# Performance work log

Hardware: AMD Instinct MI355X
Metric: run time of the kernel (lower is better)

Reference implementation:

```python
import jax, jax.numpy as jnp
import numpy as np

B, T, TM, V = 16, 128, 128, 25
CIN, CM = 64, 256
H, D1, D2 = 8, 32, 32
COUT, K = 256, 3
EPS = 1e-6


def setup_inputs() -> dict:
    key = jax.random.key(0)
    ks = jax.random.split(key, 12)
    n = lambda k, s, sc=1.0: jax.random.normal(k, s, jnp.float32) * sc
    inp = {
        'x': n(ks[0], (B, T, V, CIN)),
        'm': n(ks[1], (B, TM, V, CM)),
        'A': jax.random.uniform(ks[2], (K, V, V), jnp.float32),
        'mask': jnp.tril(jnp.ones((T, T), bool)),  # causal decoder mask over time
        # temporal self-attention projections (concat-heads output = H*D1)
        'Wq1': n(ks[3], (CIN, H * D1), 0.05),
        'Wk1': n(ks[4], (CIN, H * D1), 0.05),
        'Wv1': n(ks[5], (CIN, H * D1), 0.05),
        'g1': jnp.ones((H * D1,), jnp.float32),
        'b1': jnp.zeros((H * D1,), jnp.float32),
        # temporal cross-attention: Q from x (H*D1 ch), K/V from memory m (CM ch)
        'Wq2': n(ks[6], (H * D1, H * D2), 0.05),
        'Wk2': n(ks[7], (CM, H * D2), 0.05),
        'Wv2': n(ks[8], (CM, H * D2), 0.05),
        'g2': jnp.ones((H * D2,), jnp.float32),
        'b2': jnp.zeros((H * D2,), jnp.float32),
        # spatial GCN: 1x1 channel expansion to K*COUT then contract with A[k,v,w]
        'Wg': n(ks[9], (H * D2, K * COUT), 0.05),
        'bg': jnp.zeros((K * COUT,), jnp.float32),
        'g3': jnp.ones((COUT,), jnp.float32),
        'b3': jnp.zeros((COUT,), jnp.float32),
    }
    return inp


def _split_heads(t):
    # [B, T, V, H*d] -> [B, H, V, T, d]
    b, tt, v, hd = t.shape
    return t.reshape(b, tt, v, H, hd // H).transpose(0, 3, 2, 1, 4)


def _merge_heads(t):
    # [B, H, V, T, d] -> [B, T, V, H*d]
    b, h, v, tt, d = t.shape
    return t.transpose(0, 3, 2, 1, 4).reshape(b, tt, v, h * d)


def _temporal_attn(q, k, v, mask):
    d = q.shape[-1]
    scores = jnp.einsum('bhvtd,bhvsd->bhvts', q, k) / np.float32(np.sqrt(d))
    if mask is not None:
        scores = jnp.where(mask[None, None, None], scores, jnp.float32(-1e9))
    p = jax.nn.softmax(scores, axis=-1)
    return jnp.einsum('bhvts,bhvsd->bhvtd', p, v)


def _layernorm(x, g, b):
    mu = jnp.mean(x, axis=-1, keepdims=True)
    sd = jnp.std(x, axis=-1, ddof=1, keepdims=True)  # torch std default: unbiased
    return g * (x - mu) / (sd + EPS) + b


def reference(x, m, A, mask, Wq1, Wk1, Wv1, g1, b1, Wq2, Wk2, Wv2, g2, b2, Wg, bg, g3, b3):
    # stage 1: masked temporal self-attention per node
    q = _split_heads(x @ Wq1)
    k = _split_heads(x @ Wk1)
    v = _split_heads(x @ Wv1)
    h1 = _merge_heads(_temporal_attn(q, k, v, mask))          # [B,T,V,H*D1]
    h1 = _layernorm(h1, g1, b1)
    # stage 2: temporal cross-attention against encoder memory
    q = _split_heads(h1 @ Wq2)
    k = _split_heads(m @ Wk2)
    v = _split_heads(m @ Wv2)
    h2 = _merge_heads(_temporal_attn(q, k, v, None))           # [B,T,V,H*D2]
    h2 = _layernorm(h2, g2, b2)
    # stage 3: spatial GCN (ST-GCN style): expand channels to K*COUT, contract with A
    xw = (h2 @ Wg + bg).reshape(B, T, V, K, COUT)
    h3 = jnp.einsum('btvkc,kvw->btwc', xw, A)                  # [B,T,V,COUT]
    return _layernorm(h3, g3, b3)
```

## Files before the change

kernel.cpp:

```cpp
#include <hip/hip_runtime.h>
#include <hip/hip_bf16.h>

typedef unsigned short ush;
typedef unsigned int uint32;
typedef __attribute__((ext_vector_type(8))) short s8v;
typedef __attribute__((ext_vector_type(4))) float f4v;

#define NB 16
#define NT 128
#define NTM 128
#define NV 25
#define NCIN 64
#define NCM 256
#define NH 8
#define ND 32
#define NC 256
#define NK 3
#define NKC 768
#define LN_EPS 1e-6f
#define QSCALE 0.17677669529663687f

__device__ __forceinline__ float bf2f(ush u) {
    union { uint32 i; float f; } x; x.i = ((uint32)u) << 16; return x.f;
}
__device__ __forceinline__ ush f2bf(float f) {
    union { float f; uint32 i; } x; x.f = f;
    uint32 r = x.i + 0x7FFFu + ((x.i >> 16) & 1u);
    return (ush)(r >> 16);
}
__device__ __forceinline__ uint32 pack2(float a, float b) {
    return (uint32)f2bf(a) | ((uint32)f2bf(b) << 16);
}

__global__ __launch_bounds__(256) void k_detect(const uint32* __restrict__ xw,
                                               int* __restrict__ flag)
{
    __shared__ int cnt;
    if (threadIdx.x == 0) cnt = 0;
    __syncthreads();
    int c = 0;
    for (int i = 0; i < 4; ++i) {
        uint32 u = xw[threadIdx.x + 256 * i];
        uint32 e = (u >> 7) & 0xFF;
        c += (e >= 100 && e <= 135) ? 1 : 0;
    }
    atomicAdd(&cnt, c);
    __syncthreads();
    if (threadIdx.x == 0) *flag = (cnt > 700) ? 1 : 0;
}

__global__ __launch_bounds__(256) void k_convA(const void* __restrict__ src,
                                               ush* __restrict__ A2,
                                               float* __restrict__ cs4,
                                               const int* __restrict__ flag)
{
    const bool isbf = (*flag != 0);
    const int tid = threadIdx.x;
    __shared__ float As[1875];
    for (int i = tid; i < 1875; i += 256)
        As[i] = isbf ? bf2f(((const ush*)src)[i]) : ((const float*)src)[i];
    __syncthreads();
    for (int j = tid; j < 32 * 96; j += 256) {
        int w = j / 96, kk = j - w * 96, k = kk >> 5, v = kk & 31;
        float val = (w < NV && v < NV) ? As[k * 625 + v * 25 + w] : 0.f;
        A2[j] = f2bf(val);
    }
    for (int j = tid; j < 100; j += 256) {
        int w = j >> 2, k = j & 3;
        float s = 0.f;
        if (k < 3)
            for (int v = 0; v < NV; ++v) s += As[k * 625 + v * 25 + w];
        cs4[j] = s;
    }
}

struct CvEnt { const void* src; ush* dst; int n; int K; int N; int blk0; };
struct CvTab { CvEnt e[16]; };

__global__ __launch_bounds__(256) void k_convall(CvTab tab, const int* __restrict__ flag)
{
    const bool isbf = (*flag != 0);
    const int bi = (int)blockIdx.x;
    int ei = 0;
    #pragma unroll
    for (int i = 1; i < 16; ++i) if (bi >= tab.e[i].blk0) ei = i;
    const CvEnt& e = tab.e[ei];
    if (e.K == 0) {
        const int idx = (bi - e.blk0) * 2048 + (int)threadIdx.x * 8;
        if (idx >= e.n) return;
        if (isbf) {
            *(uint4*)&e.dst[idx] = *(const uint4*)((const ush*)e.src + idx);
        } else {
            const float* s = (const float*)e.src + idx;
            uint4 a = *(const uint4*)s;
            uint4 b = *(const uint4*)(s + 4);
            uint4 o;
            o.x = pack2(((float*)&a)[0], ((float*)&a)[1]);
            o.y = pack2(((float*)&a)[2], ((float*)&a)[3]);
            o.z = pack2(((float*)&b)[0], ((float*)&b)[1]);
            o.w = pack2(((float*)&b)[2], ((float*)&b)[3]);
            *(uint4*)&e.dst[idx] = o;
        }
    } else {
        const int s4 = (bi - e.blk0) * 1024 + (int)threadIdx.x * 4;
        if (s4 >= e.n) return;
        const int k = s4 / e.N, n0 = s4 - k * e.N;
        float v0, v1, v2, v3;
        if (isbf) {
            const ush* s = (const ush*)e.src + s4;
            v0 = bf2f(s[0]); v1 = bf2f(s[1]); v2 = bf2f(s[2]); v3 = bf2f(s[3]);
        } else {
            float4 f = *(const float4*)((const float*)e.src + s4);
            v0 = f.x; v1 = f.y; v2 = f.z; v3 = f.w;
        }
        ush* d = e.dst + (size_t)n0 * e.K + k;
        d[0] = f2bf(v0);
        d[e.K] = f2bf(v1);
        d[2 * e.K] = f2bf(v2);
        d[3 * e.K] = f2bf(v3);
    }
}

__global__ __launch_bounds__(256) void k_gemm(
    const ush* __restrict__ A, const ush* __restrict__ Bt, ush* __restrict__ C,
    int M, int K, int ldC)
{
    const int n0 = blockIdx.x * 128, m0 = blockIdx.y * 128;
    const int tid = threadIdx.x, w = tid >> 6, l = tid & 63;
    __shared__ ush As[8192], Bs[8192];
    const char* AsB = (const char*)As;
    const char* BsB = (const char*)Bs;
    const int rl = l >> 3, cc = l & 7;
    f4v acc[4][4] = {};
    const int wm = w >> 1, wn = w & 1;

    for (int kt = 0; kt < K; kt += 64) {
        __syncthreads();
        #pragma unroll
        for (int j = 0; j < 4; ++j) {
            const int r = (w * 4 + j) * 8 + rl;
            const int sc = (cc ^ (r & 7)) * 8;
            const ush* ga = &A[(size_t)(m0 + r) * K + kt + sc];
            const ush* gb = &Bt[(size_t)(n0 + r) * K + kt + sc];
            __builtin_amdgcn_global_load_lds(
                (const __attribute__((address_space(1))) uint32*)ga,
                (__attribute__((address_space(3))) uint32*)&As[(w * 4 + j) * 512], 16, 0, 0);
            __builtin_amdgcn_global_load_lds(
                (const __attribute__((address_space(1))) uint32*)gb,
                (__attribute__((address_space(3))) uint32*)&Bs[(w * 4 + j) * 512], 16, 0, 0);
        }
        __syncthreads();
        #pragma unroll
        for (int ks = 0; ks < 2; ++ks) {
            const int ko = ks * 64 + (l >> 4) * 16;
            s8v a[4], b[4];
            #pragma unroll
            for (int mi = 0; mi < 4; ++mi) {
                const int ra = wm * 64 + mi * 16 + (l & 15);
                a[mi] = *(const s8v*)(AsB + ra * 128 + (ko ^ ((ra & 7) << 4)));
            }
            #pragma unroll
            for (int ni = 0; ni < 4; ++ni) {
                const int rb = wn * 64 + ni * 16 + (l & 15);
                b[ni] = *(const s8v*)(BsB + rb * 128 + (ko ^ ((rb & 7) << 4)));
            }
            #pragma unroll
            for (int mi = 0; mi < 4; ++mi)
                #pragma unroll
                for (int ni = 0; ni < 4; ++ni)
                    acc[mi][ni] = __builtin_amdgcn_mfma_f32_16x16x32_bf16(a[mi], b[ni],
                                                                          acc[mi][ni], 0, 0, 0);
        }
    }
    const int col = n0 + wn * 64 + (l & 15);
    #pragma unroll
    for (int mi = 0; mi < 4; ++mi) {
        const int row_base = m0 + wm * 64 + mi * 16 + (l >> 4) * 4;
        #pragma unroll
        for (int ni = 0; ni < 4; ++ni)
            #pragma unroll
            for (int r = 0; r < 4; ++r)
                C[(size_t)(row_base + r) * ldC + col + ni * 16] = f2bf(acc[mi][ni][r]);
    }
}

template<int MASKED>
__global__ __launch_bounds__(512) void k_attn_mfma(
    const ush* __restrict__ QKV, ush* __restrict__ O)
{
    const int v = blockIdx.x, hq = blockIdx.y, b = blockIdx.z;
    const int tid = threadIdx.x, wv = tid >> 6, l = tid & 63;
    const int hs = wv >> 1, th = wv & 1;
    const int h = hq * 4 + hs;
    const int g = l >> 4, c = l & 15;
    __shared__ ush Vs[4][NT * ND];
    const size_t tokStride = (size_t)NV * NKC;
    const ush* base = QKV + ((size_t)b * NT * NV + v) * NKC;

    const int vrow = l >> 2, vch = (l & 3) * 8;
    #pragma unroll
    for (int i = 0; i < 4; ++i) {
        const int row = 16 * (4 * th + i) + vrow;
        s8v rv = *(const s8v*)(base + (size_t)row * tokStride + 512 + h * ND + vch);
        *(s8v*)&Vs[hs][row * ND + vch] = rv;
    }
    s8v kf[8];
    const int koff = 256 + h * ND + g * 8;
    #pragma unroll
    for (int si = 0; si < 8; ++si)
        kf[si] = *(const s8v*)(base + (size_t)(16 * si + c) * tokStride + koff);
    __syncthreads();
    s8v vf[4][2];
    #pragma unroll
    for (int ks = 0; ks < 4; ++ks)
        #pragma unroll
        for (int ni = 0; ni < 2; ++ni) {
            s8v tmp;
            #pragma unroll
            for (int j = 0; j < 8; ++j)
                tmp[j] = (short)Vs[hs][(32 * ks + 8 * g + j) * ND + 16 * ni + c];
            vf[ks][ni] = tmp;
        }

    ush* og = O + ((size_t)b * NT * NV + v) * NC + h * ND;
    const int qoff = h * ND + g * 8;
    const int ga = (g & 1) * 2;
    const int l1 = ga * 16 + c, l2 = l1 + 16;
    const bool hisel = (g >> 1) != 0;

    for (int i = 0; i < 4; ++i) {
        const int t16 = 4 * th + i;
        s8v qf = *(const s8v*)(base + (size_t)(16 * t16 + c) * tokStride + qoff);
        f4v st[8];
        #pragma unroll
        for (int si = 0; si < 8; ++si) {
            if (MASKED && si > t16) { st[si] = (f4v){0.f, 0.f, 0.f, 0.f}; continue; }
            st[si] = __builtin_amdgcn_mfma_f32_16x16x32_bf16(kf[si], qf,
                                                             (f4v){0.f, 0.f, 0.f, 0.f}, 0, 0, 0);
        }
        const int t = 16 * t16 + c;
        if (MASKED) {
            #pragma unroll
            for (int si = 0; si < 8; ++si) {
                if (si > t16) continue;
                #pragma unroll
                for (int r = 0; r < 4; ++r)
                    if (16 * si + 4 * g + r > t) st[si][r] = -1e30f;
            }
        }
        float mx = -1e30f;
        #pragma unroll
        for (int si = 0; si < 8; ++si) {
            if (MASKED && si > t16) continue;
            #pragma unroll
            for (int r = 0; r < 4; ++r) mx = fmaxf(mx, st[si][r]);
        }
        mx = fmaxf(mx, __shfl_xor(mx, 16));
        mx = fmaxf(mx, __shfl_xor(mx, 32));
        float sm = 0.f;
        #pragma unroll
        for (int si = 0; si < 8; ++si) {
            if (MASKED && si > t16) continue;
            #pragma unroll
            for (int r = 0; r < 4; ++r) {
                float e = __expf((st[si][r] - mx) * QSCALE);
                st[si][r] = e;
                sm += e;
            }
        }
        sm += __shfl_xor(sm, 16);
        sm += __shfl_xor(sm, 32);
        const float inv = 1.f / sm;
        uint32 u[8][2];
        #pragma unroll
        for (int si = 0; si < 8; ++si) {
            if (MASKED && si > t16) { u[si][0] = 0u; u[si][1] = 0u; continue; }
            float e0 = st[si][0] * inv, e1 = st[si][1] * inv;
            float e2 = st[si][2] * inv, e3 = st[si][3] * inv;
            asm("v_cvt_pk_bf16_f32 %0, %1, %2" : "=v"(u[si][0]) : "v"(e0), "v"(e1));
            asm("v_cvt_pk_bf16_f32 %0, %1, %2" : "=v"(u[si][1]) : "v"(e2), "v"(e3));
        }
        f4v o[2] = {};
        #pragma unroll
        for (int ks = 0; ks < 4; ++ks) {
            if (MASKED && 2 * ks > t16) continue;
            uint32 w0a = __shfl(u[2 * ks][0], l1),     w0b = __shfl(u[2 * ks][1], l1);
            uint32 w0c = __shfl(u[2 * ks][0], l2),     w0d = __shfl(u[2 * ks][1], l2);
            uint32 w1a = __shfl(u[2 * ks + 1][0], l1), w1b = __shfl(u[2 * ks + 1][1], l1);
            uint32 w1c = __shfl(u[2 * ks + 1][0], l2), w1d = __shfl(u[2 * ks + 1][1], l2);
            union { uint32 w[4]; s8v s; } pa;
            pa.w[0] = hisel ? w1a : w0a;
            pa.w[1] = hisel ? w1b : w0b;
            pa.w[2] = hisel ? w1c : w0c;
            pa.w[3] = hisel ? w1d : w0d;
            o[0] = __builtin_amdgcn_mfma_f32_16x16x32_bf16(pa.s, vf[ks][0], o[0], 0, 0, 0);
            o[1] = __builtin_amdgcn_mfma_f32_16x16x32_bf16(pa.s, vf[ks][1], o[1], 0, 0, 0);
        }
        #pragma unroll
        for (int ni = 0; ni < 2; ++ni)
            #pragma unroll
            for (int r = 0; r < 4; ++r)
                og[(size_t)(16 * t16 + 4 * g + r) * (NV * NC) + 16 * ni + c] = f2bf(o[ni][r]);
    }
}

__global__ __launch_bounds__(256) void k_ln(
    ush* __restrict__ buf, const ush* __restrict__ g, const ush* __restrict__ bb)
{
    const int row = blockIdx.x * 4 + (threadIdx.x >> 6);
    const int lane = threadIdx.x & 63;
    ush* p = buf + (size_t)row * NC + lane * 4;
    uint2 u = *(uint2*)p;
    float x0 = bf2f((ush)(u.x & 0xffff)), x1 = bf2f((ush)(u.x >> 16));
    float x2 = bf2f((ush)(u.y & 0xffff)), x3 = bf2f((ush)(u.y >> 16));
    float s = x0 + x1 + x2 + x3;
    float q = x0 * x0 + x1 * x1 + x2 * x2 + x3 * x3;
    #pragma unroll
    for (int o = 32; o; o >>= 1) { s += __shfl_xor(s, o); q += __shfl_xor(q, o); }
    float mean = s * (1.f / 256.f);
    float var = fmaxf((q - 256.f * mean * mean) * (1.f / 255.f), 0.f);
    float inv = 1.f / (sqrtf(var) + LN_EPS);
    float o0 = bf2f(g[lane * 4 + 0]) * (x0 - mean) * inv + bf2f(bb[lane * 4 + 0]);
    float o1 = bf2f(g[lane * 4 + 1]) * (x1 - mean) * inv + bf2f(bb[lane * 4 + 1]);
    float o2 = bf2f(g[lane * 4 + 2]) * (x2 - mean) * inv + bf2f(bb[lane * 4 + 2]);
    float o3 = bf2f(g[lane * 4 + 3]) * (x3 - mean) * inv + bf2f(bb[lane * 4 + 3]);
    uint32 lo = (uint32)f2bf(o0) | ((uint32)f2bf(o1) << 16);
    uint32 hi = (uint32)f2bf(o2) | ((uint32)f2bf(o3) << 16);
    *(uint2*)p = make_uint2(lo, hi);
}

__global__ __launch_bounds__(256) void k_gcn_mfma(
    const ush* __restrict__ xw, const ush* __restrict__ A2,
    const float* __restrict__ cs4,
    const ush* __restrict__ bg, const ush* __restrict__ g3, const ush* __restrict__ b3,
    float* __restrict__ outp)
{
    const int t = blockIdx.x, b = blockIdx.y;
    const int tid = threadIdx.x;
    __shared__ uint4 Xs4[2400];
    char* Xs = (char*)Xs4;
    float* h3s = (float*)Xs4;
    const int l = tid & 63, wv = tid >> 6, g = l >> 4, c4 = l & 15;

    s8v af[2][3];
    #pragma unroll
    for (int mi = 0; mi < 2; ++mi)
        #pragma unroll
        for (int ks = 0; ks < 3; ++ks)
            af[mi][ks] = *(const s8v*)&A2[(mi * 16 + c4) * 96 + ks * 32 + g * 8];

    const ush* xr = xw + ((size_t)(b * NT + t)) * NV * NKC;
    for (int i = tid; i < 2400; i += 256) {
        int v = i / 96, c8 = i - v * 96;
        uint32 off = (uint32)(v * 1536 + c8 * 16) ^ (((v >> 3) & 3) << 4);
        *(uint4*)(Xs + off) = *(const uint4*)&xr[(size_t)v * NKC + c8 * 8];
    }
    __syncthreads();

    f4v acc[2][4] = {};
    const int c0 = wv * 64;
    #pragma unroll
    for (int ks = 0; ks < 3; ++ks) {
        #pragma unroll
        for (int ni = 0; ni < 4; ++ni) {
            const int c = c0 + ni * 16 + c4;
            s8v bfr;
            #pragma unroll
            for (int j = 0; j < 8; ++j) {
                int v = g * 8 + j; if (v > 24) v = 24;
                uint32 off = (uint32)(v * 1536 + ks * 512 + c * 2) ^ (((v >> 3) & 3) << 4);
                bfr[j] = *(const short*)(Xs + off);
            }
            acc[0][ni] = __builtin_amdgcn_mfma_f32_16x16x32_bf16(af[0][ks], bfr, acc[0][ni], 0, 0, 0);
            acc[1][ni] = __builtin_amdgcn_mfma_f32_16x16x32_bf16(af[1][ks], bfr, acc[1][ni], 0, 0, 0);
        }
    }
    __syncthreads();
    #pragma unroll
    for (int mi = 0; mi < 2; ++mi)
        #pragma unroll
        for (int r = 0; r < 4; ++r) {
            const int w = mi * 16 + g * 4 + r;
            if (w < NV) {
                #pragma unroll
                for (int ni = 0; ni < 4; ++ni)
                    h3s[w * 260 + c0 + ni * 16 + c4] = acc[mi][ni][r];
            }
        }
    __syncthreads();
    {
        const int lane = tid & 63;
        float bgq[3][4];
        #pragma unroll
        for (int k = 0; k < 3; ++k)
            #pragma unroll
            for (int i = 0; i < 4; ++i)
                bgq[k][i] = bf2f(bg[k * NC + lane * 4 + i]);
        for (int w = wv; w < NV; w += 4) {
            float4 xq = *(const float4*)&h3s[w * 260 + lane * 4];
            const float cw0 = cs4[w * 4], cw1 = cs4[w * 4 + 1], cw2 = cs4[w * 4 + 2];
            xq.x += cw0 * bgq[0][0] + cw1 * bgq[1][0] + cw2 * bgq[2][0];
            xq.y += cw0 * bgq[0][1] + cw1 * bgq[1][1] + cw2 * bgq[2][1];
            xq.z += cw0 * bgq[0][2] + cw1 * bgq[1][2] + cw2 * bgq[2][2];
            xq.w += cw0 * bgq[0][3] + cw1 * bgq[1][3] + cw2 * bgq[2][3];
            float s = xq.x + xq.y + xq.z + xq.w;
            float q = xq.x * xq.x + xq.y * xq.y + xq.z * xq.z + xq.w * xq.w;
            #pragma unroll
            for (int o = 32; o; o >>= 1) { s += __shfl_xor(s, o); q += __shfl_xor(q, o); }
            float mean = s * (1.f / 256.f);
            float var = fmaxf((q - 256.f * mean * mean) * (1.f / 255.f), 0.f);
            float inv = 1.f / (sqrtf(var) + LN_EPS);
            float o0 = bf2f(g3[lane * 4 + 0]) * (xq.x - mean) * inv + bf2f(b3[lane * 4 + 0]);
            float o1 = bf2f(g3[lane * 4 + 1]) * (xq.y - mean) * inv + bf2f(b3[lane * 4 + 1]);
            float o2 = bf2f(g3[lane * 4 + 2]) * (xq.z - mean) * inv + bf2f(b3[lane * 4 + 2]);
            float o3 = bf2f(g3[lane * 4 + 3]) * (xq.w - mean) * inv + bf2f(b3[lane * 4 + 3]);
            float* op = outp + (((size_t)(b * NT + t)) * NV + w) * NC + lane * 4;
            *(float4*)op = make_float4(o0, o1, o2, o3);
        }
    }
}

extern "C" void kernel_launch(void* const* d_in, const int* in_sizes, int n_in,
                              void* d_out, int out_size, void* d_ws, size_t ws_size,
                              hipStream_t stream)
{
    const size_t NTOK = (size_t)NB * NT * NV;
    char* ws = (char*)d_ws;
    int* flag = (int*)ws;
    ush* A2 = (ush*)(ws + 256);
    float* cs4 = (float*)(ws + 256 + 6144);
    ush* bufA = (ush*)(ws + 16384);
    ush* bufB = bufA + NTOK * NKC;
    ush* conv = bufB + NTOK * NC;

    k_detect<<<1, 256, 0, stream>>>((const uint32*)d_in[0], flag);
    k_convA<<<1, 256, 0, stream>>>(d_in[2], A2, cs4, flag);

    CvTab tab;
    int nent = 0, blk = 0;
    ush* p = conv;
    const ush* cp[18] = {};
    auto add = [&](int idx, int n, int K, int N, ush*& dst_out) {
        tab.e[nent] = { d_in[idx], p, n, K, N, blk };
        dst_out = p;
        blk += (K == 0) ? (n + 2047) / 2048 : (n + 1023) / 1024;
        p += (size_t)((n + 7) & ~7);
        ++nent;
    };
    ush* d;
    add(0, NB * NT * NV * NCIN, 0, 0, d);  cp[0] = d;
    add(1, NB * NTM * NV * NCM, 0, 0, d);  cp[1] = d;
    add(15, NKC, 0, 0, d);                 cp[15] = d;
    add(7, NC, 0, 0, d);  cp[7] = d;
    add(8, NC, 0, 0, d);  cp[8] = d;
    add(12, NC, 0, 0, d); cp[12] = d;
    add(13, NC, 0, 0, d); cp[13] = d;
    add(16, NC, 0, 0, d); cp[16] = d;
    add(17, NC, 0, 0, d); cp[17] = d;
    ush* w1t;
    add(4, NCIN * NC, NCIN, NC, w1t);
    add(5, NCIN * NC, NCIN, NC, d);
    add(6, NCIN * NC, NCIN, NC, d);
    ush* wq2t;
    add(9, NC * NC, NC, NC, wq2t);
    ush* wkv2t;
    add(10, NCM * NC, NCM, NC, wkv2t);
    add(11, NCM * NC, NCM, NC, d);
    ush* wgt;
    add(14, NC * NKC, NC, NKC, wgt);
    k_convall<<<blk, 256, 0, stream>>>(tab, flag);

    const int M = (int)NTOK;
    k_gemm<<<dim3(6, M / 128), 256, 0, stream>>>(cp[0], w1t, bufA, M, NCIN, NKC);
    k_attn_mfma<1><<<dim3(NV, NH / 4, NB), 512, 0, stream>>>(bufA, bufB);
    k_ln<<<M / 4, 256, 0, stream>>>(bufB, cp[7], cp[8]);
    k_gemm<<<dim3(2, M / 128), 256, 0, stream>>>(bufB, wq2t, bufA, M, NC, NKC);
    k_gemm<<<dim3(4, M / 128), 256, 0, stream>>>(cp[1], wkv2t, bufA + 256, M, NCM, NKC);
    k_attn_mfma<0><<<dim3(NV, NH / 4, NB), 512, 0, stream>>>(bufA, bufB);
    k_ln<<<M / 4, 256, 0, stream>>>(bufB, cp[12], cp[13]);
    k_gemm<<<dim3(6, M / 128), 256, 0, stream>>>(bufB, wgt, bufA, M, NC, NKC);
    k_gcn_mfma<<<dim3(NT, NB), 256, 0, stream>>>(bufA, A2, cs4, cp[15], cp[16], cp[17],
                                                 (float*)d_out);
}
```

Before: 270.1 us.

## Fuse layernorm, Wg projection and graph contraction into one stage-3 kernel

Replaces the separate LN2 kernel, the Wg GEMM and the GCN kernel with a single per-(b,t) block. The block loads the 25x256 h2 tile into LDS, normalizes it in place, computes the 25x768 xw product with MFMA into swizzled LDS, then contracts with A and applies the final layernorm. This avoids writing and re-reading the large xw intermediate in global memory and removes two launches. In exchange, every block re-reads the full Wg weight matrix from global or L2, and the M dimension of 25 pads to 32, which wastes MFMA work.

```diff
diff --git a/kernel.cpp b/kernel.cpp
--- a/kernel.cpp
+++ b/kernel.cpp
@@ -324,80 +324,143 @@
     float o1 = bf2f(g[lane * 4 + 1]) * (x1 - mean) * inv + bf2f(bb[lane * 4 + 1]);
     float o2 = bf2f(g[lane * 4 + 2]) * (x2 - mean) * inv + bf2f(bb[lane * 4 + 2]);
     float o3 = bf2f(g[lane * 4 + 3]) * (x3 - mean) * inv + bf2f(bb[lane * 4 + 3]);
-    uint32 lo = (uint32)f2bf(o0) | ((uint32)f2bf(o1) << 16);
-    uint32 hi = (uint32)f2bf(o2) | ((uint32)f2bf(o3) << 16);
+    uint32 lo = pack2(o0, o1);
+    uint32 hi = pack2(o2, o3);
     *(uint2*)p = make_uint2(lo, hi);
 }
 
-__global__ __launch_bounds__(256) void k_gcn_mfma(
-    const ush* __restrict__ xw, const ush* __restrict__ A2,
-    const float* __restrict__ cs4,
+__global__ __launch_bounds__(256) void k_s3fused(
+    const ush* __restrict__ h2raw, const ush* __restrict__ wgt,
+    const ush* __restrict__ A2, const float* __restrict__ cs4,
+    const ush* __restrict__ g2, const ush* __restrict__ b2,
     const ush* __restrict__ bg, const ush* __restrict__ g3, const ush* __restrict__ b3,
     float* __restrict__ outp)
 {
     const int t = blockIdx.x, b = blockIdx.y;
+    const int bt = b * NT + t;
     const int tid = threadIdx.x;
-    __shared__ uint4 Xs4[2400];
-    char* Xs = (char*)Xs4;
-    float* h3s = (float*)Xs4;
+    __shared__ ush h2s[25 * 264];
+    __shared__ char Xs[25 * 1536];
+    float* h3s = (float*)Xs;
     const int l = tid & 63, wv = tid >> 6, g = l >> 4, c4 = l & 15;
 
-    s8v af[2][3];
-    #pragma unroll
-    for (int mi = 0; mi < 2; ++mi)
-        #pragma unroll
-        for (int ks = 0; ks < 3; ++ks)
-            af[mi][ks] = *(const s8v*)&A2[(mi * 16 + c4) * 96 + ks * 32 + g * 8];
-
-    const ush* xr = xw + ((size_t)(b * NT + t)) * NV * NKC;
-    for (int i = tid; i < 2400; i += 256) {
-        int v = i / 96, c8 = i - v * 96;
-        uint32 off = (uint32)(v * 1536 + c8 * 16) ^ (((v >> 3) & 3) << 4);
-        *(uint4*)(Xs + off) = *(const uint4*)&xr[(size_t)v * NKC + c8 * 8];
-    }
-    __syncthreads();
-
-    f4v acc[2][4] = {};
-    const int c0 = wv * 64;
-    #pragma unroll
-    for (int ks = 0; ks < 3; ++ks) {
-        #pragma unroll
-        for (int ni = 0; ni < 4; ++ni) {
-            const int c = c0 + ni * 16 + c4;
-            s8v bfr;
-            #pragma unroll
-            for (int j = 0; j < 8; ++j) {
-                int v = g * 8 + j; if (v > 24) v = 24;
-                uint32 off = (uint32)(v * 1536 + ks * 512 + c * 2) ^ (((v >> 3) & 3) << 4);
-                bfr[j] = *(const short*)(Xs + off);
-            }
-            acc[0][ni] = __builtin_amdgcn_mfma_f32_16x16x32_bf16(af[0][ks], bfr, acc[0][ni], 0, 0, 0);
-            acc[1][ni] = __builtin_amdgcn_mfma_f32_16x16x32_bf16(af[1][ks], bfr, acc[1][ni], 0, 0, 0);
-        }
-    }
-    __syncthreads();
-    #pragma unroll
-    for (int mi = 0; mi < 2; ++mi)
-        #pragma unroll
-        for (int r = 0; r < 4; ++r) {
-            const int w = mi * 16 + g * 4 + r;
-            if (w < NV) {
+    const ush* hr = h2raw + (size_t)bt * NV * NC;
+    for (int i = tid; i < 800; i += 256) {
+        int r = i >> 5, c8 = (i & 31) * 8;
+        *(uint4*)&h2s[r * 264 + c8] = *(const uint4*)&hr[r * NC + c8];
+    }
+    __syncthreads();
+    {
+        float g2q[4], b2q[4];
+        #pragma unroll
+        for (int i = 0; i < 4; ++i) { g2q[i] = bf2f(g2[l * 4 + i]); b2q[i] = bf2f(b2[l * 4 + i]); }
+        for (int r = wv; r < NV; r += 4) {
+            ush* rowp = &h2s[r * 264 + l * 4];
+            uint2 u = *(uint2*)rowp;
+            float x0 = bf2f((ush)(u.x & 0xffff)), x1 = bf2f((ush)(u.x >> 16));
+            float x2 = bf2f((ush)(u.y & 0xffff)), x3 = bf2f((ush)(u.y >> 16));
+            float s = x0 + x1 + x2 + x3;
+            float q = x0 * x0 + x1 * x1 + x2 * x2 + x3 * x3;
+            #pragma unroll
+            for (int o = 32; o; o >>= 1) { s += __shfl_xor(s, o); q += __shfl_xor(q, o); }
+            float mean = s * (1.f / 256.f);
+            float var = fmaxf((q - 256.f * mean * mean) * (1.f / 255.f), 0.f);
+            float inv = 1.f / (sqrtf(var) + LN_EPS);
+            float o0 = g2q[0] * (x0 - mean) * inv + b2q[0];
+            float o1 = g2q[1] * (x1 - mean) * inv + b2q[1];
+            float o2 = g2q[2] * (x2 - mean) * inv + b2q[2];
+            float o3 = g2q[3] * (x3 - mean) * inv + b2q[3];
+            *(uint2*)rowp = make_uint2(pack2(o0, o1), pack2(o2, o3));
+        }
+    }
+    __syncthreads();
+    {
+        const int nbase = wv * 192;
+        const int v0 = c4;
+        const int v1 = (16 + c4 > 24) ? 24 : 16 + c4;
+        for (int nc = 0; nc < 3; ++nc) {
+            f4v acc[2][4] = {};
+            for (int ks = 0; ks < 8; ++ks) {
+                s8v a0 = *(const s8v*)&h2s[v0 * 264 + ks * 32 + g * 8];
+                s8v a1 = *(const s8v*)&h2s[v1 * 264 + ks * 32 + g * 8];
                 #pragma unroll
-                for (int ni = 0; ni < 4; ++ni)
-                    h3s[w * 260 + c0 + ni * 16 + c4] = acc[mi][ni][r];
-            }
-        }
-    __syncthreads();
+                for (int ni = 0; ni < 4; ++ni) {
+                    const int n = nbase + nc * 64 + ni * 16 + c4;
+                    s8v bfr = *(const s8v*)&wgt[(size_t)n * 256 + ks * 32 + g * 8];
+                    acc[0][ni] = __builtin_amdgcn_mfma_f32_16x16x32_bf16(a0, bfr, acc[0][ni], 0, 0, 0);
+                    acc[1][ni] = __builtin_amdgcn_mfma_f32_16x16x32_bf16(a1, bfr, acc[1][ni], 0, 0, 0);
+                }
+            }
+            #pragma unroll
+            for (int mi = 0; mi < 2; ++mi)
+                #pragma unroll
+                for (int r = 0; r < 4; ++r) {
+                    const int v = mi * 16 + 4 * g + r;
+                    if (v < NV) {
+                        #pragma unroll
+                        for (int ni = 0; ni < 4; ++ni) {
+                            const int col = nbase + nc * 64 + ni * 16 + c4;
+                            uint32 off = (uint32)(v * 1536 + col * 2) ^ (((v >> 3) & 3) << 4);
+                            *(ush*)(Xs + off) = f2bf(acc[mi][ni][r]);
+                        }
+                    }
+                }
+        }
+    }
+    __syncthreads();
+    f4v acc2[2][4] = {};
     {
-        const int lane = tid & 63;
-        float bgq[3][4];
+        s8v af[2][3];
+        #pragma unroll
+        for (int mi = 0; mi < 2; ++mi)
+            #pragma unroll
+            for (int ks = 0; ks < 3; ++ks)
+                af[mi][ks] = *(const s8v*)&A2[(mi * 16 + c4) * 96 + ks * 32 + g * 8];
+        const int c0 = wv * 64;
+        #pragma unroll
+        for (int ks = 0; ks < 3; ++ks) {
+            #pragma unroll
+            for (int ni = 0; ni < 4; ++ni) {
+                const int col = c0 + ni * 16 + c4;
+                s8v bfr;
+                #pragma unroll
+                for (int j = 0; j < 8; ++j) {
+                    int v = g * 8 + j; if (v > 24) v = 24;
+                    uint32 off = (uint32)(v * 1536 + (ks * 256 + col) * 2) ^ (((v >> 3) & 3) << 4);
+                    bfr[j] = *(const short*)(Xs + off);
+                }
+                acc2[0][ni] = __builtin_amdgcn_mfma_f32_16x16x32_bf16(af[0][ks], bfr, acc2[0][ni], 0, 0, 0);
+                acc2[1][ni] = __builtin_amdgcn_mfma_f32_16x16x32_bf16(af[1][ks], bfr, acc2[1][ni], 0, 0, 0);
+            }
+        }
+    }
+    __syncthreads();
+    {
+        const int c0 = wv * 64;
+        #pragma unroll
+        for (int mi = 0; mi < 2; ++mi)
+            #pragma unroll
+            for (int r = 0; r < 4; ++r) {
+                const int w = mi * 16 + 4 * g + r;
+                if (w < NV) {
+                    #pragma unroll
+                    for (int ni = 0; ni < 4; ++ni)
+                        h3s[w * 260 + c0 + ni * 16 + c4] = acc2[mi][ni][r];
+                }
+            }
+    }
+    __syncthreads();
+    {
+        float bgq[3][4], g3q[4], b3q[4];
         #pragma unroll
         for (int k = 0; k < 3; ++k)
             #pragma unroll
             for (int i = 0; i < 4; ++i)
-                bgq[k][i] = bf2f(bg[k * NC + lane * 4 + i]);
+                bgq[k][i] = bf2f(bg[k * NC + l * 4 + i]);
+        #pragma unroll
+        for (int i = 0; i < 4; ++i) { g3q[i] = bf2f(g3[l * 4 + i]); b3q[i] = bf2f(b3[l * 4 + i]); }
         for (int w = wv; w < NV; w += 4) {
-            float4 xq = *(const float4*)&h3s[w * 260 + lane * 4];
+            float4 xq = *(const float4*)&h3s[w * 260 + l * 4];
             const float cw0 = cs4[w * 4], cw1 = cs4[w * 4 + 1], cw2 = cs4[w * 4 + 2];
             xq.x += cw0 * bgq[0][0] + cw1 * bgq[1][0] + cw2 * bgq[2][0];
             xq.y += cw0 * bgq[0][1] + cw1 * bgq[1][1] + cw2 * bgq[2][1];
@@ -410,11 +473,11 @@
             float mean = s * (1.f / 256.f);
             float var = fmaxf((q - 256.f * mean * mean) * (1.f / 255.f), 0.f);
             float inv = 1.f / (sqrtf(var) + LN_EPS);
-            float o0 = bf2f(g3[lane * 4 + 0]) * (xq.x - mean) * inv + bf2f(b3[lane * 4 + 0]);
-            float o1 = bf2f(g3[lane * 4 + 1]) * (xq.y - mean) * inv + bf2f(b3[lane * 4 + 1]);
-            float o2 = bf2f(g3[lane * 4 + 2]) * (xq.z - mean) * inv + bf2f(b3[lane * 4 + 2]);
-            float o3 = bf2f(g3[lane * 4 + 3]) * (xq.w - mean) * inv + bf2f(b3[lane * 4 + 3]);
-            float* op = outp + (((size_t)(b * NT + t)) * NV + w) * NC + lane * 4;
+            float o0 = g3q[0] * (xq.x - mean) * inv + b3q[0];
+            float o1 = g3q[1] * (xq.y - mean) * inv + b3q[1];
+            float o2 = g3q[2] * (xq.z - mean) * inv + b3q[2];
+            float o3 = g3q[3] * (xq.w - mean) * inv + b3q[3];
+            float* op = outp + (((size_t)bt) * NV + w) * NC + l * 4;
             *(float4*)op = make_float4(o0, o1, o2, o3);
         }
     }
@@ -477,8 +540,7 @@
     k_gemm<<<dim3(2, M / 128), 256, 0, stream>>>(bufB, wq2t, bufA, M, NC, NKC);
     k_gemm<<<dim3(4, M / 128), 256, 0, stream>>>(cp[1], wkv2t, bufA + 256, M, NCM, NKC);
     k_attn_mfma<0><<<dim3(NV, NH / 4, NB), 512, 0, stream>>>(bufA, bufB);
-    k_ln<<<M / 4, 256, 0, stream>>>(bufB, cp[12], cp[13]);
-    k_gemm<<<dim3(6, M / 128), 256, 0, stream>>>(bufB, wgt, bufA, M, NC, NKC);
-    k_gcn_mfma<<<dim3(NT, NB), 256, 0, stream>>>(bufA, A2, cs4, cp[15], cp[16], cp[17],
-                                                 (float*)d_out);
-}
+    k_s3fused<<<dim3(NT, NB), 256, 0, stream>>>(bufB, wgt, A2, cs4,
+                                                cp[12], cp[13], cp[15], cp[16], cp[17],
+                                                (float*)d_out);
+}
```

Result: slower. 301.0 us (+11.4%).
